# Optimization experiments

Hardware: AMD Instinct MI355X
Metric: run time of the kernel (lower is better)

Reference implementation:

```python
import jax, jax.numpy as jnp
import numpy as np

N, F, H, E, G, C = 100000, 128, 128, 640000, 512, 6
EPS = 1e-5


def setup_inputs() -> dict:
    key = jax.random.key(0)
    ks = jax.random.split(key, 20)
    def w(k, shape, fan_in):
        return jax.random.normal(k, shape, jnp.float32) * (1.0 / np.sqrt(fan_in))
    return {
        "x": jax.random.normal(ks[0], (N, F), jnp.float32),
        "edge_index": jax.random.randint(ks[1], (2, E), 0, N),
        "batch": jnp.sort(jax.random.randint(ks[2], (N,), 0, G)),
        "num_graphs": G,
        # SAGEConv1: lin_l (aggregated, with bias) + lin_r (root, no bias)
        "W1l": w(ks[3], (F, H), F), "b1l": jnp.zeros((H,), jnp.float32), "W1r": w(ks[4], (F, H), F),
        # SAGEConv2
        "W2l": w(ks[5], (H, H), H), "b2l": jnp.zeros((H,), jnp.float32), "W2r": w(ks[6], (H, H), H),
        # cluster heads
        "Wc1": w(ks[7], (H, H), H), "bc1": jnp.zeros((H,), jnp.float32),
        "Wc2": w(ks[8], (H, 2), H), "bc2": jnp.zeros((2,), jnp.float32),
        # classifier
        "Wl1": w(ks[9], (H, H), H), "bl1": jnp.zeros((H,), jnp.float32),
        "Wl2": w(ks[10], (H, C), H), "bl2": jnp.zeros((C,), jnp.float32),
    }


def _sage(x, src, dst, Wl, bl, Wr):
    # PyG SAGEConv: mean-aggregate messages x[src] at dst, then lin_l(agg) + lin_r(x)
    n = x.shape[0]
    s = jax.ops.segment_sum(x[src], dst, num_segments=n)
    cnt = jax.ops.segment_sum(jnp.ones((src.shape[0],), x.dtype), dst, num_segments=n)
    agg = s / jnp.maximum(cnt, 1.0)[:, None]
    return agg @ Wl + bl + x @ Wr


def reference(x, edge_index, batch, num_graphs,
              W1l, b1l, W1r, W2l, b2l, W2r,
              Wc1, bc1, Wc2, bc2, Wl1, bl1, Wl2, bl2):
    src, dst = edge_index[0], edge_index[1]
    h = jax.nn.relu(_sage(x, src, dst, W1l, b1l, W1r))
    h = jax.nn.relu(_sage(h, src, dst, W2l, b2l, W2r))
    # 2-way soft cluster assignment per node
    a = jax.nn.softmax(jnp.tanh(h @ Wc1 + bc1) @ Wc2 + bc2, axis=1)  # [N,2]
    g = num_graphs
    # group_features[g] = a_g^T h_g  -> per-node outer product, segment-summed by graph
    gf = jax.ops.segment_sum(a[:, :, None] * h[:, None, :], batch, num_segments=g)  # [G,2,H]
    pos = gf[:, 0, :]  # positive-cluster embedding per graph
    # new_adj[g] = a_g^T A_g a_g ; only within-graph edges appear in the per-graph adj block
    same = (batch[src] == batch[dst]).astype(h.dtype)
    contrib = same[:, None, None] * (a[src][:, :, None] * a[dst][:, None, :])  # [E,2,2]
    new_adj = jax.ops.segment_sum(contrib, batch[src], num_segments=g)  # [G,2,2]
    # F.normalize(p=1, dim=1, eps=1e-5): row-wise L1 with clamped denominator
    l1 = jnp.sum(jnp.abs(new_adj), axis=2, keepdims=True)
    norm_adj = new_adj / jnp.maximum(l1, EPS)
    diag = jnp.diagonal(norm_adj, axis1=1, axis2=2)  # [G,2]
    penalty = jnp.mean(jnp.mean((diag - 1.0) ** 2, axis=1))  # mse vs ones(2), averaged over graphs
    # NOTE: original (faithfully reproduced) takes the mean over ALL nodes, same for every graph
    graph_emb = jnp.broadcast_to(jnp.mean(h, axis=0, keepdims=True), (g, h.shape[1]))
    z = jax.nn.relu(pos @ Wl1 + bl1)  # dropout off (eval mode)
    logits = z @ Wl2 + bl2
    return (jax.nn.log_softmax(logits, axis=-1), pos, graph_emb, penalty)
```

## Files before the change

kernel.cpp:

```cpp
#include <hip/hip_runtime.h>

#define NN 100000
#define NE 640000
#define HD 128
#define NG 512
#define NC 6
#define EPSV 1e-5f
#define OCT 12500

typedef __bf16 bf16_t;
typedef bf16_t bf16x8 __attribute__((ext_vector_type(8)));
typedef float f32x4 __attribute__((ext_vector_type(4)));

__device__ __forceinline__ float b2f(unsigned int u16) {
    return __builtin_bit_cast(float, u16 << 16);
}
__device__ __forceinline__ unsigned short f2b(float f) {
    unsigned int u = __builtin_bit_cast(unsigned int, f);
    unsigned int r = (u + 0x7fffu + ((u >> 16) & 1u)) >> 16;
    return (unsigned short)r;
}

__global__ __launch_bounds__(256) void k_zero(uint4* __restrict__ p, int n16) {
    int i = blockIdx.x * 256 + threadIdx.x;
    if (i < n16) p[i] = (uint4){0u, 0u, 0u, 0u};
}

__global__ __launch_bounds__(256) void k_prep(
    const float* __restrict__ x, unsigned short* __restrict__ xb,
    const float* __restrict__ Wa, const float* __restrict__ Wb,
    const float* __restrict__ Wc, const float* __restrict__ Wd,
    const float* __restrict__ We, unsigned short* __restrict__ Wt,
    const int* __restrict__ dst, int* __restrict__ cnt)
{
    int bid = blockIdx.x;
    if (bid < 960) {
        int oct = bid & 7;
        int widx = bid >> 3;
        int lo = oct * OCT, hi = lo + OCT;
        for (int e = widx * 256 + threadIdx.x; e < NE; e += 120 * 256) {
            int d = dst[e];
            if (d >= lo && d < hi) atomicAdd(&cnt[d], 1);
        }
    } else if (bid < 7210) {
        int i = (bid - 960) * 256 + threadIdx.x;
        float4 v0 = reinterpret_cast<const float4*>(x)[i * 2];
        float4 v1 = reinterpret_cast<const float4*>(x)[i * 2 + 1];
        unsigned short u[8] = {f2b(v0.x), f2b(v0.y), f2b(v0.z), f2b(v0.w),
                               f2b(v1.x), f2b(v1.y), f2b(v1.z), f2b(v1.w)};
        reinterpret_cast<uint4*>(xb)[i] = *reinterpret_cast<uint4*>(u);
    } else {
        int i = (bid - 7210) * 256 + threadIdx.x;
        int w = i >> 14, r = i & 16383;
        int k = r >> 7, n = r & 127;
        const float* W = (w == 0) ? Wa : (w == 1) ? Wb : (w == 2) ? Wc : (w == 3) ? Wd : We;
        Wt[w * 16384 + n * HD + k] = f2b(W[k * HD + n]);
    }
}

__global__ void k_scan1(const int* __restrict__ cnt, int* __restrict__ excl,
                        int* __restrict__ bsum, int n) {
    __shared__ int sh[256];
    int i = blockIdx.x * 256 + threadIdx.x;
    int v = (i < n) ? cnt[i] : 0;
    sh[threadIdx.x] = v;
    __syncthreads();
    for (int off = 1; off < 256; off <<= 1) {
        int t = (threadIdx.x >= off) ? sh[threadIdx.x - off] : 0;
        __syncthreads();
        sh[threadIdx.x] += t;
        __syncthreads();
    }
    if (i < n) excl[i] = sh[threadIdx.x] - v;
    if (threadIdx.x == 255) bsum[blockIdx.x] = sh[255];
}

__global__ void k_scan2(int* bsum, int nb) {
    __shared__ int sh[512];
    int t = threadIdx.x;
    sh[t] = (t < nb) ? bsum[t] : 0;
    __syncthreads();
    for (int off = 1; off < 512; off <<= 1) {
        int v = (t >= off) ? sh[t - off] : 0;
        __syncthreads();
        sh[t] += v;
        __syncthreads();
    }
    if (t < nb) bsum[t] = sh[t];
}

__global__ void k_scan3(const int* __restrict__ excl, const int* __restrict__ bsum,
                        int* __restrict__ row_off, int n) {
    int i = blockIdx.x * 256 + threadIdx.x;
    if (i < n) row_off[i] = excl[i] + (blockIdx.x ? bsum[blockIdx.x - 1] : 0);
    if (i == 0) row_off[n] = NE;
}

__global__ __launch_bounds__(256) void k_fill(const int* __restrict__ src,
                                              const int* __restrict__ dst,
                                              const int* __restrict__ row_off,
                                              int* __restrict__ cnt,
                                              int* __restrict__ csr) {
    int q = blockIdx.x;
    int oct = q & 7;
    int widx = q >> 3;
    int lo = oct * OCT, hi = lo + OCT;
    for (int e = widx * 256 + threadIdx.x; e < NE; e += 120 * 256) {
        int d = dst[e];
        if (d >= lo && d < hi) {
            int p = atomicSub(&cnt[d], 1);
            csr[row_off[d] + p - 1] = src[e];
        }
    }
}

__global__ __launch_bounds__(256) void k_gather_b(const unsigned short* __restrict__ X,
                                                  const int* __restrict__ row_off,
                                                  const int* __restrict__ csr,
                                                  unsigned short* __restrict__ out) {
    int node = (blockIdx.x * blockDim.x + threadIdx.x) >> 6;
    int lane = threadIdx.x & 63;
    if (node >= NN) return;
    int beg = row_off[node], end = row_off[node + 1];
    int grp = lane >> 4;
    int sub = lane & 15;
    float accA[8] = {0.f, 0.f, 0.f, 0.f, 0.f, 0.f, 0.f, 0.f};
    float accB[8] = {0.f, 0.f, 0.f, 0.f, 0.f, 0.f, 0.f, 0.f};
    for (int j = beg; j < end; j += 8) {
        int jj0 = j + grp, jj1 = j + 4 + grp;
        if (jj0 < end) {
            int s0 = csr[jj0];
            uint4 v0 = *reinterpret_cast<const uint4*>(X + (size_t)s0 * HD + sub * 8);
            accA[0] += b2f(v0.x & 0xffffu); accA[1] += b2f(v0.x >> 16);
            accA[2] += b2f(v0.y & 0xffffu); accA[3] += b2f(v0.y >> 16);
            accA[4] += b2f(v0.z & 0xffffu); accA[5] += b2f(v0.z >> 16);
            accA[6] += b2f(v0.w & 0xffffu); accA[7] += b2f(v0.w >> 16);
        }
        if (jj1 < end) {
            int s1 = csr[jj1];
            uint4 v1 = *reinterpret_cast<const uint4*>(X + (size_t)s1 * HD + sub * 8);
            accB[0] += b2f(v1.x & 0xffffu); accB[1] += b2f(v1.x >> 16);
            accB[2] += b2f(v1.y & 0xffffu); accB[3] += b2f(v1.y >> 16);
            accB[4] += b2f(v1.z & 0xffffu); accB[5] += b2f(v1.z >> 16);
            accB[6] += b2f(v1.w & 0xffffu); accB[7] += b2f(v1.w >> 16);
        }
    }
#pragma unroll
    for (int k = 0; k < 8; ++k) {
        float a = accA[k] + accB[k];
        a += __shfl_xor(a, 16, 64);
        a += __shfl_xor(a, 32, 64);
        accA[k] = a;
    }
    if (grp == 0) {
        float inv = 1.f / fmaxf((float)(end - beg), 1.f);
        unsigned short u[8];
#pragma unroll
        for (int k = 0; k < 8; ++k) u[k] = f2b(accA[k] * inv);
        *reinterpret_cast<uint4*>(out + (size_t)node * HD + sub * 8) = *reinterpret_cast<uint4*>(u);
    }
}

__global__ __launch_bounds__(256) void mfma_dual(
    const unsigned short* __restrict__ A1, const unsigned short* __restrict__ W1t,
    const unsigned short* __restrict__ A2, const unsigned short* __restrict__ W2t,
    const float* __restrict__ bias, unsigned short* __restrict__ out, int M)
{
    __shared__ uint4 wlds[2048];
    const int wid = threadIdx.x >> 6;
    const int lane = threadIdx.x & 63;
    const int lrow = lane & 15;
    const int lkg = lane >> 4;
    const int r0 = blockIdx.x * 128 + wid * 32;

    bf16x8 a[2][2][4];
#pragma unroll
    for (int s = 0; s < 2; ++s) {
        const unsigned short* Ap = s ? A2 : A1;
#pragma unroll
        for (int g = 0; g < 2; ++g) {
            int row = r0 + g * 16 + lrow;
            row = row < M ? row : M - 1;
            const unsigned short* p = Ap + (size_t)row * HD + lkg * 8;
#pragma unroll
            for (int ks = 0; ks < 4; ++ks)
                a[s][g][ks] = *reinterpret_cast<const bf16x8*>(p + ks * 32);
        }
    }

    f32x4 acc[2][8];
#pragma unroll
    for (int t = 0; t < 8; ++t) {
        float b = bias[t * 16 + lrow];
        acc[0][t] = (f32x4){b, b, b, b};
        acc[1][t] = (f32x4){b, b, b, b};
    }

    const char* ldsb = (const char*)wlds;
#pragma unroll
    for (int s = 0; s < 2; ++s) {
        const uint4* g4 = reinterpret_cast<const uint4*>(s ? W2t : W1t);
        if (s) __syncthreads();
        for (int i = threadIdx.x; i < 2048; i += 256) {
            int di = i ^ ((i >> 4) & 7);
            wlds[di] = g4[i];
        }
        __syncthreads();
#pragma unroll
        for (int ks = 0; ks < 4; ++ks) {
#pragma unroll
            for (int t = 0; t < 8; ++t) {
                int off = (lrow * 256 + lkg * 16 + t * 4096 + ks * 64) ^ ((lrow & 7) << 4);
                bf16x8 b = *reinterpret_cast<const bf16x8*>(ldsb + off);
                acc[0][t] = __builtin_amdgcn_mfma_f32_16x16x32_bf16(a[s][0][ks], b, acc[0][t], 0, 0, 0);
                acc[1][t] = __builtin_amdgcn_mfma_f32_16x16x32_bf16(a[s][1][ks], b, acc[1][t], 0, 0, 0);
            }
        }
    }

#pragma unroll
    for (int g = 0; g < 2; ++g)
#pragma unroll
        for (int t = 0; t < 8; ++t)
#pragma unroll
            for (int r = 0; r < 4; ++r) {
                int row = r0 + g * 16 + lkg * 4 + r;
                if (row < M) {
                    float v = fmaxf(acc[g][t][r], 0.f);
                    out[(size_t)row * HD + t * 16 + lrow] = f2b(v);
                }
            }
}

__global__ __launch_bounds__(256) void mfma_attn(
    const unsigned short* __restrict__ A1, const unsigned short* __restrict__ W1t,
    const float* __restrict__ bias, const float* __restrict__ Wc2,
    const float* __restrict__ bc2, float* __restrict__ a2, int M)
{
    __shared__ uint4 wlds[2048];
    const int wid = threadIdx.x >> 6;
    const int lane = threadIdx.x & 63;
    const int lrow = lane & 15;
    const int lkg = lane >> 4;
    const int r0 = blockIdx.x * 128 + wid * 32;

    bf16x8 a[2][4];
#pragma unroll
    for (int g = 0; g < 2; ++g) {
        int row = r0 + g * 16 + lrow;
        row = row < M ? row : M - 1;
        const unsigned short* p = A1 + (size_t)row * HD + lkg * 8;
#pragma unroll
        for (int ks = 0; ks < 4; ++ks)
            a[g][ks] = *reinterpret_cast<const bf16x8*>(p + ks * 32);
    }

    f32x4 acc[2][8];
#pragma unroll
    for (int t = 0; t < 8; ++t) {
        float b = bias[t * 16 + lrow];
        acc[0][t] = (f32x4){b, b, b, b};
        acc[1][t] = (f32x4){b, b, b, b};
    }

    const uint4* g4 = reinterpret_cast<const uint4*>(W1t);
    for (int i = threadIdx.x; i < 2048; i += 256) {
        int di = i ^ ((i >> 4) & 7);
        wlds[di] = g4[i];
    }
    __syncthreads();

    const char* ldsb = (const char*)wlds;
#pragma unroll
    for (int ks = 0; ks < 4; ++ks) {
#pragma unroll
        for (int t = 0; t < 8; ++t) {
            int off = (lrow * 256 + lkg * 16 + t * 4096 + ks * 64) ^ ((lrow & 7) << 4);
            bf16x8 b = *reinterpret_cast<const bf16x8*>(ldsb + off);
            acc[0][t] = __builtin_amdgcn_mfma_f32_16x16x32_bf16(a[0][ks], b, acc[0][t], 0, 0, 0);
            acc[1][t] = __builtin_amdgcn_mfma_f32_16x16x32_bf16(a[1][ks], b, acc[1][t], 0, 0, 0);
        }
    }

    float p0[2][4] = {{0.f, 0.f, 0.f, 0.f}, {0.f, 0.f, 0.f, 0.f}};
    float p1[2][4] = {{0.f, 0.f, 0.f, 0.f}, {0.f, 0.f, 0.f, 0.f}};
#pragma unroll
    for (int t = 0; t < 8; ++t) {
        float2 wv = reinterpret_cast<const float2*>(Wc2)[t * 16 + lrow];
#pragma unroll
        for (int g = 0; g < 2; ++g)
#pragma unroll
            for (int r = 0; r < 4; ++r) {
                float tv = tanhf(acc[g][t][r]);
                p0[g][r] = fmaf(tv, wv.x, p0[g][r]);
                p1[g][r] = fmaf(tv, wv.y, p1[g][r]);
            }
    }
#pragma unroll
    for (int off = 1; off < 16; off <<= 1) {
#pragma unroll
        for (int g = 0; g < 2; ++g)
#pragma unroll
            for (int r = 0; r < 4; ++r) {
                p0[g][r] += __shfl_xor(p0[g][r], off, 64);
                p1[g][r] += __shfl_xor(p1[g][r], off, 64);
            }
    }
    if (lrow == 0) {
        float B0 = bc2[0], B1 = bc2[1];
#pragma unroll
        for (int g = 0; g < 2; ++g)
#pragma unroll
            for (int r = 0; r < 4; ++r) {
                int row = r0 + g * 16 + lkg * 4 + r;
                if (row < M) {
                    float u0 = p0[g][r] + B0, u1 = p1[g][r] + B1;
                    float m = fmaxf(u0, u1);
                    float e0 = expf(u0 - m), e1 = expf(u1 - m);
                    float inv = 1.f / (e0 + e1);
                    reinterpret_cast<float2*>(a2)[row] = (float2){e0 * inv, e1 * inv};
                }
            }
    }
}

__global__ __launch_bounds__(1024) void k_pos(const unsigned short* __restrict__ h,
                                              const float* __restrict__ a2,
                                              const int* __restrict__ batch,
                                              float* __restrict__ pos_out,
                                              float* __restrict__ csum) {
    __shared__ float4 sh[16][64];
    int g = blockIdx.x;
    int lo = 0, hi = NN;
    while (lo < hi) { int m = (lo + hi) >> 1; if (batch[m] < g) lo = m + 1; else hi = m; }
    int beg = lo;
    hi = NN;
    while (lo < hi) { int m = (lo + hi) >> 1; if (batch[m] < g + 1) lo = m + 1; else hi = m; }
    int end = lo;
    int grp = threadIdx.x >> 6;
    int lane = threadIdx.x & 63;
    float4 acc = {0.f, 0.f, 0.f, 0.f};
    for (int i = beg + grp * 2; i < end; i += 32) {
        int i1 = i + 1;
        bool ok1 = i1 < end;
        float a0 = a2[i * 2];
        unsigned int v0 = *reinterpret_cast<const unsigned int*>(h + (size_t)i * HD + lane * 2);
        float a1 = ok1 ? a2[i1 * 2] : 0.f;
        unsigned int v1 = ok1 ? *reinterpret_cast<const unsigned int*>(h + (size_t)i1 * HD + lane * 2) : 0u;
        float f0 = b2f(v0 & 0xffffu), f1 = b2f(v0 >> 16);
        float g0 = b2f(v1 & 0xffffu), g1 = b2f(v1 >> 16);
        acc.x = fmaf(a0, f0, fmaf(a1, g0, acc.x));
        acc.y = fmaf(a0, f1, fmaf(a1, g1, acc.y));
        acc.z += f0 + g0;
        acc.w += f1 + g1;
    }
    sh[grp][lane] = acc;
    __syncthreads();
    if (threadIdx.x < 64) {
        float4 s = sh[0][lane];
#pragma unroll
        for (int k = 1; k < 16; ++k) {
            float4 t = sh[k][lane];
            s.x += t.x; s.y += t.y; s.z += t.z; s.w += t.w;
        }
        reinterpret_cast<float2*>(pos_out)[g * 64 + lane] = (float2){s.x, s.y};
        atomicAdd(&csum[lane * 2], s.z);
        atomicAdd(&csum[lane * 2 + 1], s.w);
    }
}

__global__ void k_gemb(const float* __restrict__ csum, float* __restrict__ out) {
    int i = blockIdx.x * 256 + threadIdx.x;
    out[i] = csum[i & 127] * (1.f / (float)NN);
}

__global__ __launch_bounds__(256) void k_adj(const int* __restrict__ src, const int* __restrict__ dst,
                                             const int* __restrict__ batch, const float* __restrict__ a2,
                                             float* __restrict__ adj) {
    __shared__ float sh[NG * 4];
    for (int i = threadIdx.x; i < NG * 4; i += 256) sh[i] = 0.f;
    __syncthreads();
    for (int e = blockIdx.x * 256 + threadIdx.x; e < NE; e += gridDim.x * 256) {
        int s = src[e], d = dst[e];
        int bs = batch[s], bd = batch[d];
        if (bs != bd) continue;
        float a0s = a2[2 * s], a1s = a2[2 * s + 1];
        float a0d = a2[2 * d], a1d = a2[2 * d + 1];
        float* A = sh + bs * 4;
        atomicAdd(A + 0, a0s * a0d);
        atomicAdd(A + 1, a0s * a1d);
        atomicAdd(A + 2, a1s * a0d);
        atomicAdd(A + 3, a1s * a1d);
    }
    __syncthreads();
    for (int i = threadIdx.x; i < NG * 4; i += 256) {
        float v = sh[i];
        if (v != 0.f) atomicAdd(&adj[i], v);
    }
}

__global__ void k_penalty(const float* __restrict__ adj, float* __restrict__ out) {
    __shared__ float sh[512];
    int g = threadIdx.x;
    float x0 = adj[g * 4], x1 = adj[g * 4 + 1], x2 = adj[g * 4 + 2], x3 = adj[g * 4 + 3];
    float l0 = fabsf(x0) + fabsf(x1);
    float l1 = fabsf(x2) + fabsf(x3);
    float d0 = x0 / fmaxf(l0, EPSV);
    float d1 = x3 / fmaxf(l1, EPSV);
    sh[g] = 0.5f * ((d0 - 1.f) * (d0 - 1.f) + (d1 - 1.f) * (d1 - 1.f));
    __syncthreads();
    for (int off = 256; off >= 1; off >>= 1) {
        if (g < off) sh[g] += sh[g + off];
        __syncthreads();
    }
    if (g == 0) out[0] = sh[0] * (1.f / (float)NG);
}

__global__ __launch_bounds__(256) void gemm_head(
    const float* __restrict__ A, const float* __restrict__ W,
    const float* __restrict__ bias, float* __restrict__ out, int M)
{
    const int tid = threadIdx.x;
    const int w = __builtin_amdgcn_readfirstlane(tid >> 6);
    const int lane = tid & 63;
    const int r0 = blockIdx.x * 32 + w * 8;
    if (r0 >= M) return;
    const int c0 = lane, c1 = lane + 64;
    float acc0[8], acc1[8];
    const float b0 = bias[c0], b1 = bias[c1];
#pragma unroll
    for (int r = 0; r < 8; ++r) { acc0[r] = b0; acc1[r] = b1; }
    const float* Ap = A + (size_t)r0 * HD;
    for (int k4 = 0; k4 < HD / 4; ++k4) {
        float4 a[8];
#pragma unroll
        for (int r = 0; r < 8; ++r)
            a[r] = *reinterpret_cast<const float4*>(Ap + r * HD + k4 * 4);
#pragma unroll
        for (int j = 0; j < 4; ++j) {
            const int k = k4 * 4 + j;
            const float w0 = W[k * HD + c0];
            const float w1 = W[k * HD + c1];
#pragma unroll
            for (int r = 0; r < 8; ++r) {
                const float av = (j == 0) ? a[r].x : (j == 1) ? a[r].y
                               : (j == 2) ? a[r].z : a[r].w;
                acc0[r] = fmaf(av, w0, acc0[r]);
                acc1[r] = fmaf(av, w1, acc1[r]);
            }
        }
    }
#pragma unroll
    for (int r = 0; r < 8; ++r) {
        out[(size_t)(r0 + r) * HD + c0] = fmaxf(acc0[r], 0.f);
        out[(size_t)(r0 + r) * HD + c1] = fmaxf(acc1[r], 0.f);
    }
}

__global__ void k_head(const float* __restrict__ z, const float* __restrict__ Wl2,
                       const float* __restrict__ bl2, float* __restrict__ out0) {
    int g = blockIdx.x * blockDim.x + threadIdx.x;
    if (g >= NG) return;
    float l[NC];
#pragma unroll
    for (int c = 0; c < NC; ++c) l[c] = bl2[c];
    for (int k = 0; k < HD; ++k) {
        float zv = z[(size_t)g * HD + k];
#pragma unroll
        for (int c = 0; c < NC; ++c) l[c] = fmaf(zv, Wl2[k * NC + c], l[c]);
    }
    float m = l[0];
#pragma unroll
    for (int c = 1; c < NC; ++c) m = fmaxf(m, l[c]);
    float sum = 0.f;
#pragma unroll
    for (int c = 0; c < NC; ++c) sum += expf(l[c] - m);
    float lse = m + logf(sum);
#pragma unroll
    for (int c = 0; c < NC; ++c) out0[g * NC + c] = l[c] - lse;
}

extern "C" void kernel_launch(void* const* d_in, const int* in_sizes, int n_in,
                              void* d_out, int out_size, void* d_ws, size_t ws_size,
                              hipStream_t stream) {
    const float* x   = (const float*)d_in[0];
    const int*   ei  = (const int*)d_in[1];
    const int*   src = ei;
    const int*   dst = ei + NE;
    const int*   batch = (const int*)d_in[2];
    const float* W1l = (const float*)d_in[4];
    const float* b1l = (const float*)d_in[5];
    const float* W1r = (const float*)d_in[6];
    const float* W2l = (const float*)d_in[7];
    const float* b2l = (const float*)d_in[8];
    const float* W2r = (const float*)d_in[9];
    const float* Wc1 = (const float*)d_in[10];
    const float* bc1 = (const float*)d_in[11];
    const float* Wc2 = (const float*)d_in[12];
    const float* bc2 = (const float*)d_in[13];
    const float* Wl1 = (const float*)d_in[14];
    const float* bl1 = (const float*)d_in[15];
    const float* Wl2 = (const float*)d_in[16];
    const float* bl2 = (const float*)d_in[17];

    char* ws = (char*)d_ws;
    const size_t BB = (size_t)NN * HD * 2;
    unsigned short* xb   = (unsigned short*)(ws);
    unsigned short* bufA = (unsigned short*)(ws + BB);
    unsigned short* bufB = (unsigned short*)(ws + 2 * BB);
    size_t O = 3 * BB;
    int*   cnt     = (int*)(ws + O);
    float* adj     = (float*)(ws + O + 400000);
    float* csum    = (float*)(ws + O + 408192);
    int*   row_off = (int*)(ws + O + 408704);
    int*   excl    = (int*)(ws + O + 808768);
    int*   bsum    = (int*)(ws + O + 1208768);
    int*   csr     = (int*)(ws + O + 1212864);
    float* a2      = (float*)(ws + O + 3772864);
    float* zbuf    = (float*)(ws + O + 4572864);
    unsigned short* w1lt = (unsigned short*)(ws + O + 4835008);
    unsigned short* w1rt = w1lt + 16384;
    unsigned short* w2lt = w1rt + 16384;
    unsigned short* w2rt = w2lt + 16384;
    unsigned short* wc1t = w2rt + 16384;

    float* out0 = (float*)d_out;
    float* pos  = out0 + NG * NC;
    float* gemb = pos + NG * HD;
    float* pen  = gemb + NG * HD;

    k_zero<<<100, 256, 0, stream>>>((uint4*)(ws + O), 25544);
    k_prep<<<7530, 256, 0, stream>>>(x, xb, W1l, W1r, W2l, W2r, Wc1, w1lt, dst, cnt);
    k_scan1<<<391, 256, 0, stream>>>(cnt, excl, bsum, NN);
    k_scan2<<<1, 512, 0, stream>>>(bsum, 391);
    k_scan3<<<391, 256, 0, stream>>>(excl, bsum, row_off, NN);
    k_fill<<<960, 256, 0, stream>>>(src, dst, row_off, cnt, csr);

    const int GEMM_GRID = (NN + 127) / 128;
    k_gather_b<<<NN / 4, 256, 0, stream>>>(xb, row_off, csr, bufA);
    mfma_dual<<<GEMM_GRID, 256, 0, stream>>>(bufA, w1lt, xb, w1rt, b1l, bufB, NN);
    k_gather_b<<<NN / 4, 256, 0, stream>>>(bufB, row_off, csr, bufA);
    mfma_dual<<<GEMM_GRID, 256, 0, stream>>>(bufA, w2lt, bufB, w2rt, b2l, xb, NN);
    mfma_attn<<<GEMM_GRID, 256, 0, stream>>>(xb, wc1t, bc1, Wc2, bc2, a2, NN);
    k_pos<<<NG, 1024, 0, stream>>>(xb, a2, batch, pos, csum);
    k_gemb<<<NG * HD / 256, 256, 0, stream>>>(csum, gemb);
    k_adj<<<120, 256, 0, stream>>>(src, dst, batch, a2, adj);
    k_penalty<<<1, 512, 0, stream>>>(adj, pen);
    gemm_head<<<NG / 32, 256, 0, stream>>>(pos, Wl1, bl1, zbuf, NG);
    k_head<<<2, 256, 0, stream>>>(zbuf, Wl2, bl2, out0);
}
```

Baseline: 309.3 us.

## Fuse neighbor mean-gather into SAGE MFMA GEMM and merge tail kernels

Each SAGE layer's CSR mean-aggregation now happens inside the MFMA GEMM kernel, so the aggregated bf16 buffer is never written to or read back from global memory. Both weight matrices are staged together into LDS, and each wave handles 16 rows. Each lane gathers 4 k-slices per neighbor into registers, which changes the gather access pattern and adds register pressure and load imbalance across rows. Separately, the pos and adj kernels are merged into one launch, as are the gemb and penalty kernels, cutting the number of launches.

Measured after the change: 289.2 us. -6.5%, faster.

```diff
diff --git a/kernel.cpp b/kernel.cpp
--- a/kernel.cpp
+++ b/kernel.cpp
@@ -114,122 +114,135 @@
     }
 }
 
-__global__ __launch_bounds__(256) void k_gather_b(const unsigned short* __restrict__ X,
-                                                  const int* __restrict__ row_off,
-                                                  const int* __restrict__ csr,
-                                                  unsigned short* __restrict__ out) {
-    int node = (blockIdx.x * blockDim.x + threadIdx.x) >> 6;
-    int lane = threadIdx.x & 63;
-    if (node >= NN) return;
-    int beg = row_off[node], end = row_off[node + 1];
-    int grp = lane >> 4;
-    int sub = lane & 15;
-    float accA[8] = {0.f, 0.f, 0.f, 0.f, 0.f, 0.f, 0.f, 0.f};
-    float accB[8] = {0.f, 0.f, 0.f, 0.f, 0.f, 0.f, 0.f, 0.f};
-    for (int j = beg; j < end; j += 8) {
-        int jj0 = j + grp, jj1 = j + 4 + grp;
-        if (jj0 < end) {
-            int s0 = csr[jj0];
-            uint4 v0 = *reinterpret_cast<const uint4*>(X + (size_t)s0 * HD + sub * 8);
-            accA[0] += b2f(v0.x & 0xffffu); accA[1] += b2f(v0.x >> 16);
-            accA[2] += b2f(v0.y & 0xffffu); accA[3] += b2f(v0.y >> 16);
-            accA[4] += b2f(v0.z & 0xffffu); accA[5] += b2f(v0.z >> 16);
-            accA[6] += b2f(v0.w & 0xffffu); accA[7] += b2f(v0.w >> 16);
-        }
-        if (jj1 < end) {
-            int s1 = csr[jj1];
-            uint4 v1 = *reinterpret_cast<const uint4*>(X + (size_t)s1 * HD + sub * 8);
-            accB[0] += b2f(v1.x & 0xffffu); accB[1] += b2f(v1.x >> 16);
-            accB[2] += b2f(v1.y & 0xffffu); accB[3] += b2f(v1.y >> 16);
-            accB[4] += b2f(v1.z & 0xffffu); accB[5] += b2f(v1.z >> 16);
-            accB[6] += b2f(v1.w & 0xffffu); accB[7] += b2f(v1.w >> 16);
-        }
-    }
-#pragma unroll
-    for (int k = 0; k < 8; ++k) {
-        float a = accA[k] + accB[k];
-        a += __shfl_xor(a, 16, 64);
-        a += __shfl_xor(a, 32, 64);
-        accA[k] = a;
-    }
-    if (grp == 0) {
-        float inv = 1.f / fmaxf((float)(end - beg), 1.f);
-        unsigned short u[8];
-#pragma unroll
-        for (int k = 0; k < 8; ++k) u[k] = f2b(accA[k] * inv);
-        *reinterpret_cast<uint4*>(out + (size_t)node * HD + sub * 8) = *reinterpret_cast<uint4*>(u);
-    }
-}
-
-__global__ __launch_bounds__(256) void mfma_dual(
-    const unsigned short* __restrict__ A1, const unsigned short* __restrict__ W1t,
-    const unsigned short* __restrict__ A2, const unsigned short* __restrict__ W2t,
+__global__ __launch_bounds__(256) void k_sage(
+    const unsigned short* __restrict__ X,
+    const int* __restrict__ row_off, const int* __restrict__ csr,
+    const unsigned short* __restrict__ Wlt, const unsigned short* __restrict__ Wrt,
     const float* __restrict__ bias, unsigned short* __restrict__ out, int M)
 {
-    __shared__ uint4 wlds[2048];
+    __shared__ uint4 wlds[4096];
     const int wid = threadIdx.x >> 6;
     const int lane = threadIdx.x & 63;
     const int lrow = lane & 15;
     const int lkg = lane >> 4;
-    const int r0 = blockIdx.x * 128 + wid * 32;
-
-    bf16x8 a[2][2][4];
-#pragma unroll
-    for (int s = 0; s < 2; ++s) {
-        const unsigned short* Ap = s ? A2 : A1;
-#pragma unroll
-        for (int g = 0; g < 2; ++g) {
-            int row = r0 + g * 16 + lrow;
-            row = row < M ? row : M - 1;
-            const unsigned short* p = Ap + (size_t)row * HD + lkg * 8;
-#pragma unroll
-            for (int ks = 0; ks < 4; ++ks)
-                a[s][g][ks] = *reinterpret_cast<const bf16x8*>(p + ks * 32);
-        }
-    }
-
-    f32x4 acc[2][8];
+    const int r0 = blockIdx.x * 64 + wid * 16;
+
+    const uint4* gl = reinterpret_cast<const uint4*>(Wlt);
+    const uint4* gr = reinterpret_cast<const uint4*>(Wrt);
+    for (int i = threadIdx.x; i < 2048; i += 256) {
+        int di = i ^ ((i >> 4) & 7);
+        wlds[di] = gl[i];
+        wlds[2048 + di] = gr[i];
+    }
+
+    int row = r0 + lrow;
+    row = row < M ? row : M - 1;
+    int beg = row_off[row], end = row_off[row + 1];
+
+    float accg[4][8];
+#pragma unroll
+    for (int ks = 0; ks < 4; ++ks)
+#pragma unroll
+        for (int j = 0; j < 8; ++j) accg[ks][j] = 0.f;
+
+    const unsigned short* Xk = X + lkg * 8;
+    for (int j = beg; j < end; j += 2) {
+        int s0 = csr[j];
+        const unsigned short* p0 = Xk + (size_t)s0 * HD;
+        uint4 w0 = *reinterpret_cast<const uint4*>(p0);
+        uint4 w1 = *reinterpret_cast<const uint4*>(p0 + 32);
+        uint4 w2 = *reinterpret_cast<const uint4*>(p0 + 64);
+        uint4 w3 = *reinterpret_cast<const uint4*>(p0 + 96);
+        bool ok1 = (j + 1) < end;
+        int s1 = csr[ok1 ? j + 1 : j];
+        const unsigned short* p1 = Xk + (size_t)s1 * HD;
+        uint4 y0, y1, y2, y3;
+        if (ok1) {
+            y0 = *reinterpret_cast<const uint4*>(p1);
+            y1 = *reinterpret_cast<const uint4*>(p1 + 32);
+            y2 = *reinterpret_cast<const uint4*>(p1 + 64);
+            y3 = *reinterpret_cast<const uint4*>(p1 + 96);
+        }
+        accg[0][0] += b2f(w0.x & 0xffffu); accg[0][1] += b2f(w0.x >> 16);
+        accg[0][2] += b2f(w0.y & 0xffffu); accg[0][3] += b2f(w0.y >> 16);
+        accg[0][4] += b2f(w0.z & 0xffffu); accg[0][5] += b2f(w0.z >> 16);
+        accg[0][6] += b2f(w0.w & 0xffffu); accg[0][7] += b2f(w0.w >> 16);
+        accg[1][0] += b2f(w1.x & 0xffffu); accg[1][1] += b2f(w1.x >> 16);
+        accg[1][2] += b2f(w1.y & 0xffffu); accg[1][3] += b2f(w1.y >> 16);
+        accg[1][4] += b2f(w1.z & 0xffffu); accg[1][5] += b2f(w1.z >> 16);
+        accg[1][6] += b2f(w1.w & 0xffffu); accg[1][7] += b2f(w1.w >> 16);
+        accg[2][0] += b2f(w2.x & 0xffffu); accg[2][1] += b2f(w2.x >> 16);
+        accg[2][2] += b2f(w2.y & 0xffffu); accg[2][3] += b2f(w2.y >> 16);
+        accg[2][4] += b2f(w2.z & 0xffffu); accg[2][5] += b2f(w2.z >> 16);
+        accg[2][6] += b2f(w2.w & 0xffffu); accg[2][7] += b2f(w2.w >> 16);
+        accg[3][0] += b2f(w3.x & 0xffffu); accg[3][1] += b2f(w3.x >> 16);
+        accg[3][2] += b2f(w3.y & 0xffffu); accg[3][3] += b2f(w3.y >> 16);
+        accg[3][4] += b2f(w3.z & 0xffffu); accg[3][5] += b2f(w3.z >> 16);
+        accg[3][6] += b2f(w3.w & 0xffffu); accg[3][7] += b2f(w3.w >> 16);
+        if (ok1) {
+            accg[0][0] += b2f(y0.x & 0xffffu); accg[0][1] += b2f(y0.x >> 16);
+            accg[0][2] += b2f(y0.y & 0xffffu); accg[0][3] += b2f(y0.y >> 16);
+            accg[0][4] += b2f(y0.z & 0xffffu); accg[0][5] += b2f(y0.z >> 16);
+            accg[0][6] += b2f(y0.w & 0xffffu); accg[0][7] += b2f(y0.w >> 16);
+            accg[1][0] += b2f(y1.x & 0xffffu); accg[1][1] += b2f(y1.x >> 16);
+            accg[1][2] += b2f(y1.y & 0xffffu); accg[1][3] += b2f(y1.y >> 16);
+            accg[1][4] += b2f(y1.z & 0xffffu); accg[1][5] += b2f(y1.z >> 16);
+            accg[1][6] += b2f(y1.w & 0xffffu); accg[1][7] += b2f(y1.w >> 16);
+            accg[2][0] += b2f(y2.x & 0xffffu); accg[2][1] += b2f(y2.x >> 16);
+            accg[2][2] += b2f(y2.y & 0xffffu); accg[2][3] += b2f(y2.y >> 16);
+            accg[2][4] += b2f(y2.z & 0xffffu); accg[2][5] += b2f(y2.z >> 16);
+            accg[2][6] += b2f(y2.w & 0xffffu); accg[2][7] += b2f(y2.w >> 16);
+            accg[3][0] += b2f(y3.x & 0xffffu); accg[3][1] += b2f(y3.x >> 16);
+            accg[3][2] += b2f(y3.y & 0xffffu); accg[3][3] += b2f(y3.y >> 16);
+            accg[3][4] += b2f(y3.z & 0xffffu); accg[3][5] += b2f(y3.z >> 16);
+            accg[3][6] += b2f(y3.w & 0xffffu); accg[3][7] += b2f(y3.w >> 16);
+        }
+    }
+
+    float inv = 1.f / fmaxf((float)(end - beg), 1.f);
+    bf16x8 a1[4], a2f[4];
+#pragma unroll
+    for (int ks = 0; ks < 4; ++ks) {
+        unsigned short u[8];
+#pragma unroll
+        for (int j = 0; j < 8; ++j) u[j] = f2b(accg[ks][j] * inv);
+        a1[ks] = *reinterpret_cast<bf16x8*>(u);
+    }
+    const unsigned short* p2 = X + (size_t)row * HD + lkg * 8;
+#pragma unroll
+    for (int ks = 0; ks < 4; ++ks)
+        a2f[ks] = *reinterpret_cast<const bf16x8*>(p2 + ks * 32);
+
+    f32x4 acc[8];
 #pragma unroll
     for (int t = 0; t < 8; ++t) {
         float b = bias[t * 16 + lrow];
-        acc[0][t] = (f32x4){b, b, b, b};
-        acc[1][t] = (f32x4){b, b, b, b};
-    }
+        acc[t] = (f32x4){b, b, b, b};
+    }
+
+    __syncthreads();
 
     const char* ldsb = (const char*)wlds;
 #pragma unroll
-    for (int s = 0; s < 2; ++s) {
-        const uint4* g4 = reinterpret_cast<const uint4*>(s ? W2t : W1t);
-        if (s) __syncthreads();
-        for (int i = threadIdx.x; i < 2048; i += 256) {
-            int di = i ^ ((i >> 4) & 7);
-            wlds[di] = g4[i];
-        }
-        __syncthreads();
-#pragma unroll
-        for (int ks = 0; ks < 4; ++ks) {
-#pragma unroll
-            for (int t = 0; t < 8; ++t) {
-                int off = (lrow * 256 + lkg * 16 + t * 4096 + ks * 64) ^ ((lrow & 7) << 4);
-                bf16x8 b = *reinterpret_cast<const bf16x8*>(ldsb + off);
-                acc[0][t] = __builtin_amdgcn_mfma_f32_16x16x32_bf16(a[s][0][ks], b, acc[0][t], 0, 0, 0);
-                acc[1][t] = __builtin_amdgcn_mfma_f32_16x16x32_bf16(a[s][1][ks], b, acc[1][t], 0, 0, 0);
-            }
-        }
-    }
-
-#pragma unroll
-    for (int g = 0; g < 2; ++g)
-#pragma unroll
-        for (int t = 0; t < 8; ++t)
-#pragma unroll
-            for (int r = 0; r < 4; ++r) {
-                int row = r0 + g * 16 + lkg * 4 + r;
-                if (row < M) {
-                    float v = fmaxf(acc[g][t][r], 0.f);
-                    out[(size_t)row * HD + t * 16 + lrow] = f2b(v);
-                }
-            }
+    for (int ks = 0; ks < 4; ++ks) {
+#pragma unroll
+        for (int t = 0; t < 8; ++t) {
+            int off = (lrow * 256 + lkg * 16 + t * 4096 + ks * 64) ^ ((lrow & 7) << 4);
+            bf16x8 bl = *reinterpret_cast<const bf16x8*>(ldsb + off);
+            bf16x8 br = *reinterpret_cast<const bf16x8*>(ldsb + 32768 + off);
+            acc[t] = __builtin_amdgcn_mfma_f32_16x16x32_bf16(a1[ks], bl, acc[t], 0, 0, 0);
+            acc[t] = __builtin_amdgcn_mfma_f32_16x16x32_bf16(a2f[ks], br, acc[t], 0, 0, 0);
+        }
+    }
+
+#pragma unroll
+    for (int t = 0; t < 8; ++t)
+#pragma unroll
+        for (int r = 0; r < 4; ++r) {
+            int orow = r0 + lkg * 4 + r;
+            if (orow < M)
+                out[(size_t)orow * HD + t * 16 + lrow] = f2b(fmaxf(acc[t][r], 0.f));
+        }
 }
 
 __global__ __launch_bounds__(256) void mfma_attn(
@@ -324,96 +337,102 @@
     }
 }
 
-__global__ __launch_bounds__(1024) void k_pos(const unsigned short* __restrict__ h,
-                                              const float* __restrict__ a2,
-                                              const int* __restrict__ batch,
-                                              float* __restrict__ pos_out,
-                                              float* __restrict__ csum) {
+__global__ __launch_bounds__(1024) void k_posadj(const unsigned short* __restrict__ h,
+                                                 const float* __restrict__ a2,
+                                                 const int* __restrict__ batch,
+                                                 const int* __restrict__ src,
+                                                 const int* __restrict__ dst,
+                                                 float* __restrict__ pos_out,
+                                                 float* __restrict__ csum,
+                                                 float* __restrict__ adj) {
     __shared__ float4 sh[16][64];
-    int g = blockIdx.x;
-    int lo = 0, hi = NN;
-    while (lo < hi) { int m = (lo + hi) >> 1; if (batch[m] < g) lo = m + 1; else hi = m; }
-    int beg = lo;
-    hi = NN;
-    while (lo < hi) { int m = (lo + hi) >> 1; if (batch[m] < g + 1) lo = m + 1; else hi = m; }
-    int end = lo;
-    int grp = threadIdx.x >> 6;
-    int lane = threadIdx.x & 63;
-    float4 acc = {0.f, 0.f, 0.f, 0.f};
-    for (int i = beg + grp * 2; i < end; i += 32) {
-        int i1 = i + 1;
-        bool ok1 = i1 < end;
-        float a0 = a2[i * 2];
-        unsigned int v0 = *reinterpret_cast<const unsigned int*>(h + (size_t)i * HD + lane * 2);
-        float a1 = ok1 ? a2[i1 * 2] : 0.f;
-        unsigned int v1 = ok1 ? *reinterpret_cast<const unsigned int*>(h + (size_t)i1 * HD + lane * 2) : 0u;
-        float f0 = b2f(v0 & 0xffffu), f1 = b2f(v0 >> 16);
-        float g0 = b2f(v1 & 0xffffu), g1 = b2f(v1 >> 16);
-        acc.x = fmaf(a0, f0, fmaf(a1, g0, acc.x));
-        acc.y = fmaf(a0, f1, fmaf(a1, g1, acc.y));
-        acc.z += f0 + g0;
-        acc.w += f1 + g1;
-    }
-    sh[grp][lane] = acc;
-    __syncthreads();
-    if (threadIdx.x < 64) {
-        float4 s = sh[0][lane];
-#pragma unroll
-        for (int k = 1; k < 16; ++k) {
-            float4 t = sh[k][lane];
-            s.x += t.x; s.y += t.y; s.z += t.z; s.w += t.w;
-        }
-        reinterpret_cast<float2*>(pos_out)[g * 64 + lane] = (float2){s.x, s.y};
-        atomicAdd(&csum[lane * 2], s.z);
-        atomicAdd(&csum[lane * 2 + 1], s.w);
-    }
-}
-
-__global__ void k_gemb(const float* __restrict__ csum, float* __restrict__ out) {
-    int i = blockIdx.x * 256 + threadIdx.x;
-    out[i] = csum[i & 127] * (1.f / (float)NN);
-}
-
-__global__ __launch_bounds__(256) void k_adj(const int* __restrict__ src, const int* __restrict__ dst,
-                                             const int* __restrict__ batch, const float* __restrict__ a2,
-                                             float* __restrict__ adj) {
-    __shared__ float sh[NG * 4];
-    for (int i = threadIdx.x; i < NG * 4; i += 256) sh[i] = 0.f;
-    __syncthreads();
-    for (int e = blockIdx.x * 256 + threadIdx.x; e < NE; e += gridDim.x * 256) {
-        int s = src[e], d = dst[e];
-        int bs = batch[s], bd = batch[d];
-        if (bs != bd) continue;
-        float a0s = a2[2 * s], a1s = a2[2 * s + 1];
-        float a0d = a2[2 * d], a1d = a2[2 * d + 1];
-        float* A = sh + bs * 4;
-        atomicAdd(A + 0, a0s * a0d);
-        atomicAdd(A + 1, a0s * a1d);
-        atomicAdd(A + 2, a1s * a0d);
-        atomicAdd(A + 3, a1s * a1d);
-    }
-    __syncthreads();
-    for (int i = threadIdx.x; i < NG * 4; i += 256) {
-        float v = sh[i];
-        if (v != 0.f) atomicAdd(&adj[i], v);
-    }
-}
-
-__global__ void k_penalty(const float* __restrict__ adj, float* __restrict__ out) {
-    __shared__ float sh[512];
-    int g = threadIdx.x;
-    float x0 = adj[g * 4], x1 = adj[g * 4 + 1], x2 = adj[g * 4 + 2], x3 = adj[g * 4 + 3];
-    float l0 = fabsf(x0) + fabsf(x1);
-    float l1 = fabsf(x2) + fabsf(x3);
-    float d0 = x0 / fmaxf(l0, EPSV);
-    float d1 = x3 / fmaxf(l1, EPSV);
-    sh[g] = 0.5f * ((d0 - 1.f) * (d0 - 1.f) + (d1 - 1.f) * (d1 - 1.f));
-    __syncthreads();
-    for (int off = 256; off >= 1; off >>= 1) {
-        if (g < off) sh[g] += sh[g + off];
-        __syncthreads();
-    }
-    if (g == 0) out[0] = sh[0] * (1.f / (float)NG);
+    __shared__ float shadj[NG * 4];
+    int bid = blockIdx.x;
+    if (bid < NG) {
+        int g = bid;
+        int lo = 0, hi = NN;
+        while (lo < hi) { int m = (lo + hi) >> 1; if (batch[m] < g) lo = m + 1; else hi = m; }
+        int beg = lo;
+        hi = NN;
+        while (lo < hi) { int m = (lo + hi) >> 1; if (batch[m] < g + 1) lo = m + 1; else hi = m; }
+        int end = lo;
+        int grp = threadIdx.x >> 6;
+        int lane = threadIdx.x & 63;
+        float4 acc = {0.f, 0.f, 0.f, 0.f};
+        for (int i = beg + grp * 2; i < end; i += 32) {
+            int i1 = i + 1;
+            bool ok1 = i1 < end;
+            float a0 = a2[i * 2];
+            unsigned int v0 = *reinterpret_cast<const unsigned int*>(h + (size_t)i * HD + lane * 2);
+            float a1 = ok1 ? a2[i1 * 2] : 0.f;
+            unsigned int v1 = ok1 ? *reinterpret_cast<const unsigned int*>(h + (size_t)i1 * HD + lane * 2) : 0u;
+            float f0 = b2f(v0 & 0xffffu), f1 = b2f(v0 >> 16);
+            float g0 = b2f(v1 & 0xffffu), g1 = b2f(v1 >> 16);
+            acc.x = fmaf(a0, f0, fmaf(a1, g0, acc.x));
+            acc.y = fmaf(a0, f1, fmaf(a1, g1, acc.y));
+            acc.z += f0 + g0;
+            acc.w += f1 + g1;
+        }
+        sh[grp][lane] = acc;
+        __syncthreads();
+        if (threadIdx.x < 64) {
+            float4 s = sh[0][lane];
+#pragma unroll
+            for (int k = 1; k < 16; ++k) {
+                float4 t = sh[k][lane];
+                s.x += t.x; s.y += t.y; s.z += t.z; s.w += t.w;
+            }
+            reinterpret_cast<float2*>(pos_out)[g * 64 + lane] = (float2){s.x, s.y};
+            atomicAdd(&csum[lane * 2], s.z);
+            atomicAdd(&csum[lane * 2 + 1], s.w);
+        }
+    } else {
+        for (int i = threadIdx.x; i < NG * 4; i += 1024) shadj[i] = 0.f;
+        __syncthreads();
+        for (int e = (bid - NG) * 1024 + threadIdx.x; e < NE; e += 120 * 1024) {
+            int s = src[e], d = dst[e];
+            int bs = batch[s], bd = batch[d];
+            if (bs != bd) continue;
+            float a0s = a2[2 * s], a1s = a2[2 * s + 1];
+            float a0d = a2[2 * d], a1d = a2[2 * d + 1];
+            float* A = shadj + bs * 4;
+            atomicAdd(A + 0, a0s * a0d);
+            atomicAdd(A + 1, a0s * a1d);
+            atomicAdd(A + 2, a1s * a0d);
+            atomicAdd(A + 3, a1s * a1d);
+        }
+        __syncthreads();
+        for (int i = threadIdx.x; i < NG * 4; i += 1024) {
+            float v = shadj[i];
+            if (v != 0.f) atomicAdd(&adj[i], v);
+        }
+    }
+}
+
+__global__ __launch_bounds__(512) void k_tail(const float* __restrict__ csum,
+                                              float* __restrict__ gemb_out,
+                                              const float* __restrict__ adj,
+                                              float* __restrict__ pen) {
+    int bid = blockIdx.x;
+    if (bid < 128) {
+        int i = bid * 512 + threadIdx.x;
+        gemb_out[i] = csum[i & 127] * (1.f / (float)NN);
+    } else {
+        __shared__ float sh[512];
+        int g = threadIdx.x;
+        float x0 = adj[g * 4], x1 = adj[g * 4 + 1], x2 = adj[g * 4 + 2], x3 = adj[g * 4 + 3];
+        float l0 = fabsf(x0) + fabsf(x1);
+        float l1 = fabsf(x2) + fabsf(x3);
+        float d0 = x0 / fmaxf(l0, EPSV);
+        float d1 = x3 / fmaxf(l1, EPSV);
+        sh[g] = 0.5f * ((d0 - 1.f) * (d0 - 1.f) + (d1 - 1.f) * (d1 - 1.f));
+        __syncthreads();
+        for (int off = 256; off >= 1; off >>= 1) {
+            if (g < off) sh[g] += sh[g + off];
+            __syncthreads();
+        }
+        if (g == 0) pen[0] = sh[0] * (1.f / (float)NG);
+    }
 }
 
 __global__ __launch_bounds__(256) void gemm_head(
@@ -506,9 +525,8 @@
     char* ws = (char*)d_ws;
     const size_t BB = (size_t)NN * HD * 2;
     unsigned short* xb   = (unsigned short*)(ws);
-    unsigned short* bufA = (unsigned short*)(ws + BB);
-    unsigned short* bufB = (unsigned short*)(ws + 2 * BB);
-    size_t O = 3 * BB;
+    unsigned short* bufB = (unsigned short*)(ws + BB);
+    size_t O = 2 * BB;
     int*   cnt     = (int*)(ws + O);
     float* adj     = (float*)(ws + O + 400000);
     float* csum    = (float*)(ws + O + 408192);
@@ -536,16 +554,12 @@
     k_scan3<<<391, 256, 0, stream>>>(excl, bsum, row_off, NN);
     k_fill<<<960, 256, 0, stream>>>(src, dst, row_off, cnt, csr);
 
-    const int GEMM_GRID = (NN + 127) / 128;
-    k_gather_b<<<NN / 4, 256, 0, stream>>>(xb, row_off, csr, bufA);
-    mfma_dual<<<GEMM_GRID, 256, 0, stream>>>(bufA, w1lt, xb, w1rt, b1l, bufB, NN);
-    k_gather_b<<<NN / 4, 256, 0, stream>>>(bufB, row_off, csr, bufA);
-    mfma_dual<<<GEMM_GRID, 256, 0, stream>>>(bufA, w2lt, bufB, w2rt, b2l, xb, NN);
-    mfma_attn<<<GEMM_GRID, 256, 0, stream>>>(xb, wc1t, bc1, Wc2, bc2, a2, NN);
-    k_pos<<<NG, 1024, 0, stream>>>(xb, a2, batch, pos, csum);
-    k_gemb<<<NG * HD / 256, 256, 0, stream>>>(csum, gemb);
-    k_adj<<<120, 256, 0, stream>>>(src, dst, batch, a2, adj);
-    k_penalty<<<1, 512, 0, stream>>>(adj, pen);
+    const int SAGE_GRID = (NN + 63) / 64;
+    k_sage<<<SAGE_GRID, 256, 0, stream>>>(xb, row_off, csr, w1lt, w1rt, b1l, bufB, NN);
+    k_sage<<<SAGE_GRID, 256, 0, stream>>>(bufB, row_off, csr, w2lt, w2rt, b2l, xb, NN);
+    mfma_attn<<<(NN + 127) / 128, 256, 0, stream>>>(xb, wc1t, bc1, Wc2, bc2, a2, NN);
+    k_posadj<<<NG + 120, 1024, 0, stream>>>(xb, a2, batch, src, dst, pos, csum, adj);
+    k_tail<<<129, 512, 0, stream>>>(csum, gemb, adj, pen);
     gemm_head<<<NG / 32, 256, 0, stream>>>(pos, Wl1, bl1, zbuf, NG);
     k_head<<<2, 256, 0, stream>>>(zbuf, Wl2, bl2, out0);
 }
```
